# Kernel optimization log

Hardware: AMD Instinct MI355X
Metric: run time of the kernel (lower is better)

The kernel has to match this reference:

```python
import jax, jax.numpy as jnp
import numpy as np

DIM = 768
HEADS = 16
HEAD_DIM = DIM // HEADS  # 48


def setup_inputs() -> dict:
    key = jax.random.key(0)
    ks = jax.random.split(key, 9)
    s = 1.0 / np.sqrt(DIM)
    inp = {
        "x": jax.random.normal(ks[0], (4, 2048, DIM), dtype=jnp.float32),
        "Wq": jax.random.uniform(ks[1], (DIM, DIM), jnp.float32, -s, s),
        "bq": jax.random.uniform(ks[2], (DIM,), jnp.float32, -s, s),
        "Wk": jax.random.uniform(ks[3], (DIM, DIM), jnp.float32, -s, s),
        "bk": jax.random.uniform(ks[4], (DIM,), jnp.float32, -s, s),
        "Wv": jax.random.uniform(ks[5], (DIM, DIM), jnp.float32, -s, s),
        "bv": jax.random.uniform(ks[6], (DIM,), jnp.float32, -s, s),
        "Wo": jax.random.uniform(ks[7], (DIM, DIM), jnp.float32, -s, s),
        "bo": jax.random.uniform(ks[8], (DIM,), jnp.float32, -s, s),
    }
    return inp


def reference(x, Wq, bq, Wk, bk, Wv, bv, Wo, bo):
    B, S, _ = x.shape
    # torch nn.Linear: y = x @ W.T + b
    q = x @ Wq.T + bq
    k = x @ Wk.T + bk
    v = x @ Wv.T + bv
    # split heads: (B, H, S, Dh)
    q = q.reshape(B, S, HEADS, HEAD_DIM).transpose(0, 2, 1, 3)
    k = k.reshape(B, S, HEADS, HEAD_DIM).transpose(0, 2, 1, 3)
    v = v.reshape(B, S, HEADS, HEAD_DIM).transpose(0, 2, 1, 3)
    score = jnp.einsum("bhqd,bhkd->bhqk", q, k) / jnp.sqrt(jnp.float32(HEAD_DIM))
    attn = jax.nn.softmax(score, axis=-1)
    out = jnp.einsum("bhqk,bhkd->bhqd", attn, v)
    out = out.transpose(0, 2, 1, 3).reshape(B, S, DIM)
    return out @ Wo.T + bo
```

## Files before the change

### kernel.cpp

```cpp
#include <hip/hip_runtime.h>

#define DIM 768
#define SEQ 2048
#define NB 4
#define NH 16
#define DH 48
#define DP 64
#define BHN (NB*NH)
#define MTOK (NB*SEQ)

typedef __attribute__((ext_vector_type(8))) short bf16x8;
typedef __attribute__((ext_vector_type(4))) float f32x4;
typedef __attribute__((ext_vector_type(4))) unsigned int u32x4;

__device__ __forceinline__ unsigned short f32_to_bf16(float f) {
    union { float f; unsigned int u; } v; v.f = f;
    unsigned int r = v.u + 0x7fff + ((v.u >> 16) & 1);
    return (unsigned short)(r >> 16);
}

#if __has_builtin(__builtin_amdgcn_exp2f)
#define EXP2F(x) __builtin_amdgcn_exp2f(x)
#else
#define EXP2F(x) exp2f(x)
#endif

#define GL_LDS16(g, l) __builtin_amdgcn_global_load_lds( \
    (const __attribute__((address_space(1))) void*)(g),  \
    (__attribute__((address_space(3))) void*)(l), 16, 0, 0)

__global__ void cvt_f32_bf16(const float* __restrict__ src, unsigned short* __restrict__ dst, int n) {
    int i = (blockIdx.x * blockDim.x + threadIdx.x) * 4;
    if (i + 3 < n) {
        const float4 v = *(const float4*)(src + i);
        ushort4 o;
        o.x = f32_to_bf16(v.x); o.y = f32_to_bf16(v.y);
        o.z = f32_to_bf16(v.z); o.w = f32_to_bf16(v.w);
        *(ushort4*)(dst + i) = o;
    }
}

__global__ void cvt4_f32_bf16(const float* __restrict__ a, const float* __restrict__ b,
                              const float* __restrict__ c, const float* __restrict__ d,
                              unsigned short* __restrict__ dst, int n_each) {
    const float* srcs[4] = {a, b, c, d};
    const float* src = srcs[blockIdx.y];
    unsigned short* out = dst + blockIdx.y * n_each;
    int i = (blockIdx.x * blockDim.x + threadIdx.x) * 4;
    if (i + 3 < n_each) {
        const float4 v = *(const float4*)(src + i);
        ushort4 o;
        o.x = f32_to_bf16(v.x); o.y = f32_to_bf16(v.y);
        o.z = f32_to_bf16(v.z); o.w = f32_to_bf16(v.w);
        *(ushort4*)(out + i) = o;
    }
}

#define BK 32

__global__ __launch_bounds__(256) void qkv_gemm(
    const unsigned short* __restrict__ xb,
    const unsigned short* __restrict__ wb,
    const float* __restrict__ bq, const float* __restrict__ bk, const float* __restrict__ bv,
    unsigned short* __restrict__ Qb, unsigned short* __restrict__ Kb, unsigned short* __restrict__ Vt)
{
    const int z = blockIdx.z;
    const unsigned short* W = wb + z * (DIM * DIM);
    const float* bias = (z == 0) ? bq : (z == 1) ? bk : bv;
    const int row0 = blockIdx.x * 128;
    const int col0 = blockIdx.y * 128;

    __shared__ __align__(16) short As[128 * BK];
    __shared__ __align__(16) short Bs[128 * BK];

    const int tid = threadIdx.x;
    const int lane = tid & 63;
    const int w = tid >> 6;
    const int wy = w >> 1, wx = w & 1;
    const int l15 = lane & 15, quad = lane >> 4;
    const int lr = lane >> 2;
    const int lco = (lane & 3) * 8;

    f32x4 acc[4][4];
    for (int mi = 0; mi < 4; ++mi) for (int ni = 0; ni < 4; ++ni)
        for (int r = 0; r < 4; ++r) acc[mi][ni][r] = 0.f;

    for (int kt = 0; kt < DIM / BK; ++kt) {
        #pragma unroll
        for (int j = 0; j < 2; ++j) {
            const int c = w * 2 + j;
            GL_LDS16(&xb[(row0 + c * 16 + lr) * DIM + kt * BK + lco], &As[c * 512]);
            GL_LDS16(&W [(col0 + c * 16 + lr) * DIM + kt * BK + lco], &Bs[c * 512]);
        }
        __syncthreads();
        bf16x8 af[4], bfr[4];
        #pragma unroll
        for (int mi = 0; mi < 4; ++mi)
            af[mi] = *(const bf16x8*)&As[(wy * 64 + mi * 16 + l15) * BK + quad * 8];
        #pragma unroll
        for (int ni = 0; ni < 4; ++ni)
            bfr[ni] = *(const bf16x8*)&Bs[(wx * 64 + ni * 16 + l15) * BK + quad * 8];
        #pragma unroll
        for (int mi = 0; mi < 4; ++mi)
            #pragma unroll
            for (int ni = 0; ni < 4; ++ni)
                acc[mi][ni] = __builtin_amdgcn_mfma_f32_16x16x32_bf16(af[mi], bfr[ni], acc[mi][ni], 0, 0, 0);
        __syncthreads();
    }

    const float qscale = 0.14433756729740643f * 1.4426950408889634f;

    if (z == 2) {
        #pragma unroll
        for (int mi = 0; mi < 4; ++mi) {
            #pragma unroll
            for (int ni = 0; ni < 4; ++ni) {
                int col = col0 + wx * 64 + ni * 16 + l15;
                int h = col / DH, d = col - h * DH;
                int row = row0 + wy * 64 + mi * 16 + quad * 4;
                int b = row >> 11, s = row & 2047;
                float bi = bias[col];
                union { ushort4 v; unsigned short e[4]; } pk;
                #pragma unroll
                for (int r = 0; r < 4; ++r)
                    pk.e[r] = f32_to_bf16(acc[mi][ni][r] + bi);
                *(ushort4*)&Vt[((b * NH + h) * DP + d) * SEQ + s] = pk.v;
            }
        }
    } else {
        #pragma unroll
        for (int mi = 0; mi < 4; ++mi) {
            #pragma unroll
            for (int ni = 0; ni < 4; ++ni) {
                #pragma unroll
                for (int r = 0; r < 4; ++r) {
                    int row = row0 + wy * 64 + mi * 16 + quad * 4 + r;
                    int col = col0 + wx * 64 + ni * 16 + l15;
                    float v = acc[mi][ni][r] + bias[col];
                    int b = row >> 11, s = row & 2047;
                    int h = col / DH, d = col - h * DH;
                    int bh = b * NH + h;
                    if (z == 0) Qb[(bh * SEQ + s) * DP + d] = f32_to_bf16(v * qscale);
                    else        Kb[(bh * SEQ + s) * DP + d] = f32_to_bf16(v);
                }
            }
        }
    }
}

__global__ __launch_bounds__(256) void out_gemm(
    const unsigned short* __restrict__ ab,
    const unsigned short* __restrict__ Wo,
    const float* __restrict__ bo,
    float* __restrict__ out)
{
    const int row0 = blockIdx.x * 128;
    const int col0 = blockIdx.y * 128;

    __shared__ __align__(16) short As[128 * BK];
    __shared__ __align__(16) short Bs[128 * BK];

    const int tid = threadIdx.x;
    const int lane = tid & 63;
    const int w = tid >> 6;
    const int wy = w >> 1, wx = w & 1;
    const int l15 = lane & 15, quad = lane >> 4;
    const int lr = lane >> 2;
    const int lco = (lane & 3) * 8;

    f32x4 acc[4][4];
    for (int mi = 0; mi < 4; ++mi) for (int ni = 0; ni < 4; ++ni)
        for (int r = 0; r < 4; ++r) acc[mi][ni][r] = 0.f;

    for (int kt = 0; kt < DIM / BK; ++kt) {
        #pragma unroll
        for (int j = 0; j < 2; ++j) {
            const int c = w * 2 + j;
            GL_LDS16(&ab[(row0 + c * 16 + lr) * DIM + kt * BK + lco], &As[c * 512]);
            GL_LDS16(&Wo[(col0 + c * 16 + lr) * DIM + kt * BK + lco], &Bs[c * 512]);
        }
        __syncthreads();
        bf16x8 af[4], bfr[4];
        #pragma unroll
        for (int mi = 0; mi < 4; ++mi)
            af[mi] = *(const bf16x8*)&As[(wy * 64 + mi * 16 + l15) * BK + quad * 8];
        #pragma unroll
        for (int ni = 0; ni < 4; ++ni)
            bfr[ni] = *(const bf16x8*)&Bs[(wx * 64 + ni * 16 + l15) * BK + quad * 8];
        #pragma unroll
        for (int mi = 0; mi < 4; ++mi)
            #pragma unroll
            for (int ni = 0; ni < 4; ++ni)
                acc[mi][ni] = __builtin_amdgcn_mfma_f32_16x16x32_bf16(af[mi], bfr[ni], acc[mi][ni], 0, 0, 0);
        __syncthreads();
    }

    #pragma unroll
    for (int mi = 0; mi < 4; ++mi)
        #pragma unroll
        for (int ni = 0; ni < 4; ++ni)
            #pragma unroll
            for (int r = 0; r < 4; ++r) {
                int row = row0 + wy * 64 + mi * 16 + quad * 4 + r;
                int col = col0 + wx * 64 + ni * 16 + l15;
                out[row * DIM + col] = acc[mi][ni][r] + bo[col];
            }
}

__device__ __forceinline__ int keyperm(int a) {
    return (a & 32) + ((a & 12) << 1) + ((a & 16) >> 2) + (a & 3);
}

__global__ __launch_bounds__(256) void attn_kernel(
    const unsigned short* __restrict__ Qb,
    const unsigned short* __restrict__ Kb,
    const unsigned short* __restrict__ Vt,
    unsigned short* __restrict__ Ob)
{
    const int bh = blockIdx.x;
    const int tile = blockIdx.y;
    const int tid = threadIdx.x;
    const int w = tid >> 6;
    const int lane = tid & 63;
    const int l15 = lane & 15, quad = lane >> 4;

    const unsigned short* Qh = Qb + bh * SEQ * DP;
    const unsigned short* Kh = Kb + bh * SEQ * DP;
    const unsigned short* Vh = Vt + bh * DP * SEQ;
    const int q0 = tile * 128 + w * 32;

    __shared__ __align__(16) short Ks[2][64 * 64];
    __shared__ __align__(16) short Vs[2][48 * 64];

    bf16x8 aq[2][2];
    #pragma unroll
    for (int m = 0; m < 2; ++m)
        #pragma unroll
        for (int ks = 0; ks < 2; ++ks)
            aq[m][ks] = *(const bf16x8*)&Qh[(q0 + m * 16 + l15) * DP + ks * 32 + quad * 8];
    if (quad >= 2) {
        const bf16x8 z8 = {0, 0, 0, 0, 0, 0, 0, 0};
        #pragma unroll
        for (int m = 0; m < 2; ++m) aq[m][1] = z8;
    }

    f32x4 o[2][3];
    #pragma unroll
    for (int m = 0; m < 2; ++m) for (int ni = 0; ni < 3; ++ni)
        for (int r = 0; r < 4; ++r) o[m][ni][r] = 0.f;
    float ls[2][2];
    #pragma unroll
    for (int m = 0; m < 2; ++m) { ls[m][0] = 0.f; ls[m][1] = 0.f; }

    const f32x4 FZ = {0.f, 0.f, 0.f, 0.f};

    const int lr3 = lane >> 3, pcc = lane & 7;
    const int swz8 = (pcc ^ lr3) * 8;
    int kso[2], vso[2];
    #pragma unroll
    for (int j = 0; j < 2; ++j) {
        const int c = w * 2 + j;
        const int ra = c * 8 + lr3;
        kso[j] = keyperm(ra) * DP + swz8;
        vso[j] = ra * SEQ + swz8;
    }
    const bool vld = (w < 3);

    #pragma unroll
    for (int j = 0; j < 2; ++j) {
        GL_LDS16(&Kh[kso[j]], &Ks[0][(w * 2 + j) * 512]);
        if (vld) GL_LDS16(&Vh[vso[j]], &Vs[0][(w * 2 + j) * 512]);
    }

    for (int kt = 0; kt < SEQ / 64; ++kt) {
        const int cur = kt & 1;
        __syncthreads();
        if (kt + 1 < SEQ / 64) {
            const int k0n = (kt + 1) * 64;
            #pragma unroll
            for (int j = 0; j < 2; ++j) {
                GL_LDS16(&Kh[k0n * DP + kso[j]], &Ks[cur ^ 1][(w * 2 + j) * 512]);
                if (vld) GL_LDS16(&Vh[k0n + vso[j]], &Vs[cur ^ 1][(w * 2 + j) * 512]);
            }
        }

        f32x4 sc[2][4];
        __builtin_amdgcn_s_setprio(1);
        #pragma unroll
        for (int ks = 0; ks < 2; ++ks) {
            bf16x8 ak[4];
            #pragma unroll
            for (int n = 0; n < 4; ++n)
                ak[n] = *(const bf16x8*)&Ks[cur][(n * 16 + l15) * 64 + (((ks * 4 + quad) ^ (l15 & 7)) * 8)];
            #pragma unroll
            for (int n = 0; n < 4; ++n) {
                sc[0][n] = __builtin_amdgcn_mfma_f32_16x16x32_bf16(ak[n], aq[0][ks], ks ? sc[0][n] : FZ, 0, 0, 0);
                sc[1][n] = __builtin_amdgcn_mfma_f32_16x16x32_bf16(ak[n], aq[1][ks], ks ? sc[1][n] : FZ, 0, 0, 0);
            }
        }
        __builtin_amdgcn_s_setprio(0);

        union { u32x4 u; bf16x8 h; } bp[2][2];
        #pragma unroll
        for (int mi = 0; mi < 2; ++mi) {
            #pragma unroll
            for (int ks = 0; ks < 2; ++ks) {
                #pragma unroll
                for (int w2 = 0; w2 < 4; ++w2) {
                    const int j0 = 2 * w2, j1 = 2 * w2 + 1;
                    float p0 = EXP2F(sc[mi][2 * ks + (j0 >> 2)][j0 & 3]);
                    float p1 = EXP2F(sc[mi][2 * ks + (j1 >> 2)][j1 & 3]);
                    ls[mi][w2 & 1] += (p0 + p1);
                    bp[mi][ks].u[w2] = __builtin_amdgcn_perm(__float_as_uint(p1), __float_as_uint(p0), 0x07060302u);
                }
            }
        }

        __builtin_amdgcn_s_setprio(1);
        #pragma unroll
        for (int ks = 0; ks < 2; ++ks) {
            bf16x8 av[3];
            #pragma unroll
            for (int mt = 0; mt < 3; ++mt)
                av[mt] = *(const bf16x8*)&Vs[cur][(mt * 16 + l15) * 64 + (((ks * 4 + quad) ^ (l15 & 7)) * 8)];
            #pragma unroll
            for (int mt = 0; mt < 3; ++mt) {
                o[0][mt] = __builtin_amdgcn_mfma_f32_16x16x32_bf16(av[mt], bp[0][ks].h, o[0][mt], 0, 0, 0);
                o[1][mt] = __builtin_amdgcn_mfma_f32_16x16x32_bf16(av[mt], bp[1][ks].h, o[1][mt], 0, 0, 0);
            }
        }
        __builtin_amdgcn_s_setprio(0);
    }

    const int b = bh >> 4, h = bh & 15;
    #pragma unroll
    for (int m = 0; m < 2; ++m) {
        float lsum = ls[m][0] + ls[m][1];
        lsum += __shfl_xor(lsum, 16);
        lsum += __shfl_xor(lsum, 32);
        float inv = 1.f / lsum;
        int token = b * SEQ + q0 + m * 16 + l15;
        #pragma unroll
        for (int mt = 0; mt < 3; ++mt) {
            union { ushort4 v; unsigned short e[4]; } pk;
            #pragma unroll
            for (int r = 0; r < 4; ++r)
                pk.e[r] = f32_to_bf16(o[m][mt][r] * inv);
            *(ushort4*)&Ob[token * DIM + h * DH + mt * 16 + quad * 4] = pk.v;
        }
    }
}

extern "C" void kernel_launch(void* const* d_in, const int* in_sizes, int n_in,
                              void* d_out, int out_size, void* d_ws, size_t ws_size,
                              hipStream_t stream) {
    const float* x  = (const float*)d_in[0];
    const float* Wq = (const float*)d_in[1]; const float* bq = (const float*)d_in[2];
    const float* Wk = (const float*)d_in[3]; const float* bk = (const float*)d_in[4];
    const float* Wv = (const float*)d_in[5]; const float* bv = (const float*)d_in[6];
    const float* Wo = (const float*)d_in[7]; const float* bo = (const float*)d_in[8];

    unsigned char* ws = (unsigned char*)d_ws;
    unsigned short* xb = (unsigned short*)(ws);
    unsigned short* wb = (unsigned short*)(ws + 12582912);
    unsigned short* Qb = (unsigned short*)(ws + 17301504);
    unsigned short* Kb = (unsigned short*)(ws + 34078720);
    unsigned short* Vt = (unsigned short*)(ws + 50855936);
    unsigned short* Ob = (unsigned short*)(ws + 67633152);

    cvt_f32_bf16<<<6144, 256, 0, stream>>>(x, xb, MTOK * DIM);
    cvt4_f32_bf16<<<dim3(576, 4), 256, 0, stream>>>(Wq, Wk, Wv, Wo, wb, DIM * DIM);

    qkv_gemm<<<dim3(MTOK / 128, DIM / 128, 3), 256, 0, stream>>>(xb, wb, bq, bk, bv, Qb, Kb, Vt);
    attn_kernel<<<dim3(BHN, SEQ / 128), 256, 0, stream>>>(Qb, Kb, Vt, Ob);
    out_gemm<<<dim3(MTOK / 128, DIM / 128), 256, 0, stream>>>(Ob, wb + 3 * DIM * DIM, bo, (float*)d_out);
}
```

Measured before the change: 229.3 us.

## Double per-warp query rows in attention and unroll K/V loop by two

Each warp now handles 64 query rows instead of 32, so every K/V tile loaded into LDS is reused across twice as many queries and the grid halves. The key loop is manually unrolled by two with compile-time buffer indices, K and V fragments are loaded from LDS once per step and reused across two query pairs, and the barrier moves to the end of each step. The swizzle computation is also generalised to use the row index. This raises register pressure (more accumulators and Q fragments) and halves the block count, which may reduce occupancy and parallelism on the device.

```diff
diff --git a/kernel.cpp b/kernel.cpp
--- a/kernel.cpp
+++ b/kernel.cpp
@@ -227,40 +227,40 @@
     const unsigned short* Qh = Qb + bh * SEQ * DP;
     const unsigned short* Kh = Kb + bh * SEQ * DP;
     const unsigned short* Vh = Vt + bh * DP * SEQ;
-    const int q0 = tile * 128 + w * 32;
+    const int q0 = tile * 256 + w * 64;
 
     __shared__ __align__(16) short Ks[2][64 * 64];
     __shared__ __align__(16) short Vs[2][48 * 64];
 
-    bf16x8 aq[2][2];
-    #pragma unroll
-    for (int m = 0; m < 2; ++m)
+    bf16x8 aq[4][2];
+    #pragma unroll
+    for (int m = 0; m < 4; ++m)
         #pragma unroll
         for (int ks = 0; ks < 2; ++ks)
             aq[m][ks] = *(const bf16x8*)&Qh[(q0 + m * 16 + l15) * DP + ks * 32 + quad * 8];
     if (quad >= 2) {
         const bf16x8 z8 = {0, 0, 0, 0, 0, 0, 0, 0};
         #pragma unroll
-        for (int m = 0; m < 2; ++m) aq[m][1] = z8;
-    }
-
-    f32x4 o[2][3];
-    #pragma unroll
-    for (int m = 0; m < 2; ++m) for (int ni = 0; ni < 3; ++ni)
+        for (int m = 0; m < 4; ++m) aq[m][1] = z8;
+    }
+
+    f32x4 o[4][3];
+    #pragma unroll
+    for (int m = 0; m < 4; ++m) for (int ni = 0; ni < 3; ++ni)
         for (int r = 0; r < 4; ++r) o[m][ni][r] = 0.f;
-    float ls[2][2];
-    #pragma unroll
-    for (int m = 0; m < 2; ++m) { ls[m][0] = 0.f; ls[m][1] = 0.f; }
+    float ls[4][2];
+    #pragma unroll
+    for (int m = 0; m < 4; ++m) { ls[m][0] = 0.f; ls[m][1] = 0.f; }
 
     const f32x4 FZ = {0.f, 0.f, 0.f, 0.f};
 
     const int lr3 = lane >> 3, pcc = lane & 7;
-    const int swz8 = (pcc ^ lr3) * 8;
     int kso[2], vso[2];
     #pragma unroll
     for (int j = 0; j < 2; ++j) {
         const int c = w * 2 + j;
         const int ra = c * 8 + lr3;
+        const int swz8 = ((pcc ^ (ra & 7)) * 8);
         kso[j] = keyperm(ra) * DP + swz8;
         vso[j] = ra * SEQ + swz8;
     }
@@ -271,70 +271,77 @@
         GL_LDS16(&Kh[kso[j]], &Ks[0][(w * 2 + j) * 512]);
         if (vld) GL_LDS16(&Vh[vso[j]], &Vs[0][(w * 2 + j) * 512]);
     }
-
-    for (int kt = 0; kt < SEQ / 64; ++kt) {
-        const int cur = kt & 1;
-        __syncthreads();
-        if (kt + 1 < SEQ / 64) {
-            const int k0n = (kt + 1) * 64;
-            #pragma unroll
-            for (int j = 0; j < 2; ++j) {
-                GL_LDS16(&Kh[k0n * DP + kso[j]], &Ks[cur ^ 1][(w * 2 + j) * 512]);
-                if (vld) GL_LDS16(&Vh[k0n + vso[j]], &Vs[cur ^ 1][(w * 2 + j) * 512]);
-            }
-        }
-
-        f32x4 sc[2][4];
-        __builtin_amdgcn_s_setprio(1);
-        #pragma unroll
-        for (int ks = 0; ks < 2; ++ks) {
-            bf16x8 ak[4];
-            #pragma unroll
-            for (int n = 0; n < 4; ++n)
-                ak[n] = *(const bf16x8*)&Ks[cur][(n * 16 + l15) * 64 + (((ks * 4 + quad) ^ (l15 & 7)) * 8)];
-            #pragma unroll
-            for (int n = 0; n < 4; ++n) {
-                sc[0][n] = __builtin_amdgcn_mfma_f32_16x16x32_bf16(ak[n], aq[0][ks], ks ? sc[0][n] : FZ, 0, 0, 0);
-                sc[1][n] = __builtin_amdgcn_mfma_f32_16x16x32_bf16(ak[n], aq[1][ks], ks ? sc[1][n] : FZ, 0, 0, 0);
-            }
-        }
-        __builtin_amdgcn_s_setprio(0);
-
-        union { u32x4 u; bf16x8 h; } bp[2][2];
-        #pragma unroll
-        for (int mi = 0; mi < 2; ++mi) {
-            #pragma unroll
-            for (int ks = 0; ks < 2; ++ks) {
-                #pragma unroll
-                for (int w2 = 0; w2 < 4; ++w2) {
-                    const int j0 = 2 * w2, j1 = 2 * w2 + 1;
-                    float p0 = EXP2F(sc[mi][2 * ks + (j0 >> 2)][j0 & 3]);
-                    float p1 = EXP2F(sc[mi][2 * ks + (j1 >> 2)][j1 & 3]);
-                    ls[mi][w2 & 1] += (p0 + p1);
-                    bp[mi][ks].u[w2] = __builtin_amdgcn_perm(__float_as_uint(p1), __float_as_uint(p0), 0x07060302u);
-                }
-            }
-        }
-
-        __builtin_amdgcn_s_setprio(1);
-        #pragma unroll
-        for (int ks = 0; ks < 2; ++ks) {
-            bf16x8 av[3];
-            #pragma unroll
-            for (int mt = 0; mt < 3; ++mt)
-                av[mt] = *(const bf16x8*)&Vs[cur][(mt * 16 + l15) * 64 + (((ks * 4 + quad) ^ (l15 & 7)) * 8)];
-            #pragma unroll
-            for (int mt = 0; mt < 3; ++mt) {
-                o[0][mt] = __builtin_amdgcn_mfma_f32_16x16x32_bf16(av[mt], bp[0][ks].h, o[0][mt], 0, 0, 0);
-                o[1][mt] = __builtin_amdgcn_mfma_f32_16x16x32_bf16(av[mt], bp[1][ks].h, o[1][mt], 0, 0, 0);
-            }
-        }
-        __builtin_amdgcn_s_setprio(0);
+    __syncthreads();
+
+#define ATTN_STEP(B, KT) do { \
+    if ((KT) + 1 < SEQ / 64) { \
+        const int k0n = ((KT) + 1) * 64; \
+        _Pragma("unroll") \
+        for (int j = 0; j < 2; ++j) { \
+            GL_LDS16(&Kh[k0n * DP + kso[j]], &Ks[(B) ^ 1][(w * 2 + j) * 512]); \
+            if (vld) GL_LDS16(&Vh[k0n + vso[j]], &Vs[(B) ^ 1][(w * 2 + j) * 512]); \
+        } \
+    } \
+    bf16x8 ak0[4], ak1[4]; \
+    _Pragma("unroll") \
+    for (int n = 0; n < 4; ++n) { \
+        ak0[n] = *(const bf16x8*)&Ks[B][(n * 16 + l15) * 64 + ((quad ^ (l15 & 7)) * 8)]; \
+        ak1[n] = *(const bf16x8*)&Ks[B][(n * 16 + l15) * 64 + (((4 + quad) ^ (l15 & 7)) * 8)]; \
+    } \
+    bf16x8 av[2][3]; \
+    _Pragma("unroll") \
+    for (int ks = 0; ks < 2; ++ks) \
+        _Pragma("unroll") \
+        for (int mt = 0; mt < 3; ++mt) \
+            av[ks][mt] = *(const bf16x8*)&Vs[B][(mt * 16 + l15) * 64 + (((ks * 4 + quad) ^ (l15 & 7)) * 8)]; \
+    _Pragma("unroll") \
+    for (int mp = 0; mp < 2; ++mp) { \
+        const int m0 = 2 * mp, m1 = 2 * mp + 1; \
+        f32x4 sc[2][4]; \
+        _Pragma("unroll") \
+        for (int n = 0; n < 4; ++n) { \
+            sc[0][n] = __builtin_amdgcn_mfma_f32_16x16x32_bf16(ak0[n], aq[m0][0], FZ, 0, 0, 0); \
+            sc[1][n] = __builtin_amdgcn_mfma_f32_16x16x32_bf16(ak0[n], aq[m1][0], FZ, 0, 0, 0); \
+        } \
+        _Pragma("unroll") \
+        for (int n = 0; n < 4; ++n) { \
+            sc[0][n] = __builtin_amdgcn_mfma_f32_16x16x32_bf16(ak1[n], aq[m0][1], sc[0][n], 0, 0, 0); \
+            sc[1][n] = __builtin_amdgcn_mfma_f32_16x16x32_bf16(ak1[n], aq[m1][1], sc[1][n], 0, 0, 0); \
+        } \
+        union { u32x4 u; bf16x8 h; } bp[2][2]; \
+        _Pragma("unroll") \
+        for (int mi = 0; mi < 2; ++mi) { \
+            _Pragma("unroll") \
+            for (int ks = 0; ks < 2; ++ks) { \
+                _Pragma("unroll") \
+                for (int w2 = 0; w2 < 4; ++w2) { \
+                    const int j0 = 2 * w2, j1 = 2 * w2 + 1; \
+                    float p0 = EXP2F(sc[mi][2 * ks + (j0 >> 2)][j0 & 3]); \
+                    float p1 = EXP2F(sc[mi][2 * ks + (j1 >> 2)][j1 & 3]); \
+                    ls[2 * mp + mi][w2 & 1] += (p0 + p1); \
+                    bp[mi][ks].u[w2] = __builtin_amdgcn_perm(__float_as_uint(p1), __float_as_uint(p0), 0x07060302u); \
+                } \
+            } \
+        } \
+        _Pragma("unroll") \
+        for (int ks = 0; ks < 2; ++ks) \
+            _Pragma("unroll") \
+            for (int mt = 0; mt < 3; ++mt) { \
+                o[m0][mt] = __builtin_amdgcn_mfma_f32_16x16x32_bf16(av[ks][mt], bp[0][ks].h, o[m0][mt], 0, 0, 0); \
+                o[m1][mt] = __builtin_amdgcn_mfma_f32_16x16x32_bf16(av[ks][mt], bp[1][ks].h, o[m1][mt], 0, 0, 0); \
+            } \
+    } \
+    __syncthreads(); \
+} while (0)
+
+    for (int kt = 0; kt < SEQ / 64; kt += 2) {
+        ATTN_STEP(0, kt);
+        ATTN_STEP(1, kt + 1);
     }
 
     const int b = bh >> 4, h = bh & 15;
     #pragma unroll
-    for (int m = 0; m < 2; ++m) {
+    for (int m = 0; m < 4; ++m) {
         float lsum = ls[m][0] + ls[m][1];
         lsum += __shfl_xor(lsum, 16);
         lsum += __shfl_xor(lsum, 32);
@@ -372,6 +379,6 @@
     cvt4_f32_bf16<<<dim3(576, 4), 256, 0, stream>>>(Wq, Wk, Wv, Wo, wb, DIM * DIM);
 
     qkv_gemm<<<dim3(MTOK / 128, DIM / 128, 3), 256, 0, stream>>>(xb, wb, bq, bk, bv, Qb, Kb, Vt);
-    attn_kernel<<<dim3(BHN, SEQ / 128), 256, 0, stream>>>(Qb, Kb, Vt, Ob);
+    attn_kernel<<<dim3(BHN, SEQ / 256), 256, 0, stream>>>(Qb, Kb, Vt, Ob);
     out_gemm<<<dim3(MTOK / 128, DIM / 128), 256, 0, stream>>>(Ob, wb + 3 * DIM * DIM, bo, (float*)d_out);
 }
```

After: 247.9 us. 1.08x slower.
